# Kernel optimization log

Hardware: AMD Instinct MI355X
Metric: run time of the kernel (lower is better)

## Reference

```python
import jax, jax.numpy as jnp
import numpy as np

B, T_DIM, N, D, HID, NH = 2, 512, 6, 32, 128, 4
HD = HID // NH  # 32
GH = max(32, D)  # gater hidden = 32
FD = 128  # final_dim
EPS = 1e-5


def _ln(x, w, b):
    mu = jnp.mean(x, axis=-1, keepdims=True)
    var = jnp.var(x, axis=-1, keepdims=True)
    return (x - mu) * jax.lax.rsqrt(var + EPS) * w + b


def setup_inputs() -> dict:
    key = jax.random.key(0)
    ks = jax.random.split(key, 16)
    s_d = 1.0 / np.sqrt(D)
    s_h = 1.0 / np.sqrt(HID)
    s_g = 1.0 / np.sqrt(GH)
    return {
        "per_t_forces": jax.random.normal(ks[0], (B, T_DIM, N, D), jnp.float32),
        # gater: LayerNorm(D) -> Linear(D,GH) -> SiLU -> Linear(GH,1) (bias zero-init)
        "g_ln_w": jnp.ones((D,), jnp.float32),
        "g_ln_b": jnp.zeros((D,), jnp.float32),
        "g_w1": jax.random.uniform(ks[1], (D, GH), jnp.float32, -s_d, s_d),
        "g_b1": jax.random.uniform(ks[2], (GH,), jnp.float32, -s_d, s_d),
        "g_w2": jax.random.uniform(ks[3], (GH, 1), jnp.float32, -s_g, s_g),
        "g_b2": jnp.zeros((1,), jnp.float32),
        # QKV / out projections
        "q_w": jax.random.uniform(ks[4], (D, HID), jnp.float32, -s_d, s_d),
        "q_b": jax.random.uniform(ks[5], (HID,), jnp.float32, -s_d, s_d),
        "k_w": jax.random.uniform(ks[6], (D, HID), jnp.float32, -s_d, s_d),
        "k_b": jax.random.uniform(ks[7], (HID,), jnp.float32, -s_d, s_d),
        "v_w": jax.random.uniform(ks[8], (D, HID), jnp.float32, -s_d, s_d),
        "v_b": jax.random.uniform(ks[9], (HID,), jnp.float32, -s_d, s_d),
        "o_w": jax.random.uniform(ks[10], (HID, HID), jnp.float32, -s_h, s_h),
        "o_b": jax.random.uniform(ks[11], (HID,), jnp.float32, -s_h, s_h),
        # final: LayerNorm(HID) -> Linear(HID,FD) -> SiLU
        "f_ln_w": jnp.ones((HID,), jnp.float32),
        "f_ln_b": jnp.zeros((HID,), jnp.float32),
        "f_w": jax.random.uniform(ks[12], (HID, FD), jnp.float32, -s_h, s_h),
        "f_b": jax.random.uniform(ks[13], (FD,), jnp.float32, -s_h, s_h),
        "T": T_DIM,
    }


def reference(per_t_forces, g_ln_w, g_ln_b, g_w1, g_b1, g_w2, g_b2,
              q_w, q_b, k_w, k_b, v_w, v_b, o_w, o_b,
              f_ln_w, f_ln_b, f_w, f_b, T):
    b, tt, n, d = per_t_forces.shape
    L = T * n
    x = per_t_forces.reshape(b, L, d)

    # per-force learned gating
    h = jax.nn.silu(_ln(x, g_ln_w, g_ln_b) @ g_w1 + g_b1)
    gates = jax.nn.sigmoid((h @ g_w2 + g_b2)[..., 0])  # [B, L]
    g = gates[..., None]

    # gated QKV
    Q = (x @ q_w + q_b) * g
    K = (x @ k_w + k_b) * g
    V = (x @ v_w + v_b) * g

    Qh = Q.reshape(b, L, NH, HD)
    Kh = K.reshape(b, L, NH, HD)
    Vh = V.reshape(b, L, NH, HD)

    scale = 1.0 / np.sqrt(HD)
    scores = jnp.einsum("bihd,bjhd->bhij", Qh, Kh) * scale  # [B,NH,L,L]

    # block-causal over time: token j masked out if its time block > time of i
    t_idx = jnp.arange(L) // n
    mask = t_idx[None, :] > t_idx[:, None]  # [L, L], True = masked
    scores = jnp.where(mask[None, None], -jnp.inf, scores)

    A = jnp.maximum(jax.nn.softmax(scores, axis=-1), 1e-9)
    attn = jnp.einsum("bhij,bjhd->bihd", A, Vh).reshape(b, L, HID)

    out = attn @ o_w + o_b                     # [B, L, HID]
    per_t = out.reshape(b, T, n, HID).mean(axis=2)  # mean-pool over forces
    final = jax.nn.silu(_ln(per_t, f_ln_w, f_ln_b) @ f_w + f_b)  # [B, T, FD]
    return final
```

## Files before the change

### kernel.cpp

```cpp
#include <hip/hip_runtime.h>
#include <hip/hip_bf16.h>

#define BB   2
#define TT   512
#define NF   6
#define DD   32
#define HIDD 128
#define NHH  4
#define HDD  32
#define GHH  32
#define FDD  128
#define LL   (TT*NF)
#define EPSF 1e-5f
#define NQT16 (LL/16)

#define NCHC 8
#define CCH  384
#define VPAD 8

typedef __attribute__((ext_vector_type(8))) short  bf16x8;
typedef __attribute__((ext_vector_type(4))) float  f32x4;

#define MFMA16x16x32(a,b,c) __builtin_amdgcn_mfma_f32_16x16x32_bf16(a,b,c,0,0,0)

__device__ __forceinline__ unsigned short bfh(float f) {
    union { __hip_bfloat16 b; unsigned short u; } cv;
    cv.b = __float2bfloat16(f);
    return cv.u;
}
__device__ __forceinline__ float bff(unsigned short u) {
    return __uint_as_float(((unsigned)u) << 16);
}
__device__ __forceinline__ unsigned pk_bf16(float a, float b) {
    union { __hip_bfloat162 h2; unsigned u; } cv;
    cv.h2 = __float22bfloat162_rn(make_float2(a, b));
    return cv.u;
}
__device__ __forceinline__ bf16x8 ld8(const unsigned short* p) {
    return *reinterpret_cast<const bf16x8*>(p);
}

__device__ __forceinline__ float fexp2(float x) {
#if __has_builtin(__builtin_amdgcn_exp2f)
    return __builtin_amdgcn_exp2f(x);
#else
    return exp2f(x);
#endif
}

struct Frags {
    bf16x8 k0, k1;
    bf16x8 k2, k3;
    bf16x8 v0, v1, v2, v3;
};

__device__ __forceinline__ void load_tile_lds(
    const unsigned short* ldsK, const unsigned short* ldsV,
    int j0loc, int kloc0, int kloc1, int quad, int rr, Frags& f)
{
    const int kX0 = (j0loc + kloc0) * HDD + quad * 8;
    const int kX1 = (j0loc + kloc1) * HDD + quad * 8;
    f.k0 = ld8(ldsK + kX0);
    f.k1 = ld8(ldsK + kX1);
    f.k2 = ld8(ldsK + kX0 + 32 * HDD);
    f.k3 = ld8(ldsK + kX1 + 32 * HDD);
    const int vX = j0loc + quad * 8, vY = vX + 32;
    const int vr0 = rr * (CCH + VPAD), vr1 = (rr + 16) * (CCH + VPAD);
    f.v0 = ld8(ldsV + vr0 + vX);
    f.v1 = ld8(ldsV + vr1 + vX);
    f.v2 = ld8(ldsV + vr0 + vY);
    f.v3 = ld8(ldsV + vr1 + vY);
}

__device__ __forceinline__ void compute_tile(
    const Frags& f, const bf16x8 qfh, const bf16x8 qfl,
    int j0, int jminw, int jend, int quad,
    float& m, float& l, f32x4& o0, f32x4& o1)
{
    const f32x4 z = {0.f, 0.f, 0.f, 0.f};
    f32x4 s0 = MFMA16x16x32(f.k0, qfh, z);
    f32x4 s1 = MFMA16x16x32(f.k1, qfh, z);
    f32x4 s2 = MFMA16x16x32(f.k2, qfh, z);
    f32x4 s3 = MFMA16x16x32(f.k3, qfh, z);
    s0 = MFMA16x16x32(f.k0, qfl, s0);
    s1 = MFMA16x16x32(f.k1, qfl, s1);
    s2 = MFMA16x16x32(f.k2, qfl, s2);
    s3 = MFMA16x16x32(f.k3, qfl, s3);

    float e[16], mx, ls, corr;
    if (j0 + 64 <= jminw) {
        f32x4 m4 = s0;
        #pragma unroll
        for (int r2 = 0; r2 < 4; r2++)
            m4[r2] = fmaxf(fmaxf(m4[r2], s1[r2]), fmaxf(s2[r2], s3[r2]));
        mx = fmaxf(fmaxf(m4[0], m4[1]), fmaxf(m4[2], m4[3]));
        mx = fmaxf(mx, __shfl_xor(mx, 16));
        mx = fmaxf(mx, __shfl_xor(mx, 32));
        mx = fmaxf(m, mx);
        corr = fexp2(m - mx); m = mx;
        ls = 0.f;
        #pragma unroll
        for (int r2 = 0; r2 < 4; r2++) {
            float e0 = fexp2(s0[r2] - mx);
            float e1 = fexp2(s1[r2] - mx);
            float e2 = fexp2(s2[r2] - mx);
            float e3 = fexp2(s3[r2] - mx);
            e[r2] = e0; e[4 + r2] = e1; e[8 + r2] = e2; e[12 + r2] = e3;
            ls += (e0 + e1) + (e2 + e3);
        }
    } else {
        const int je = jend - j0;
        const int k0 = 8 * quad;
        float t[16];
        #pragma unroll
        for (int r2 = 0; r2 < 4; r2++) {
            t[r2]      = (k0 + r2          < je) ? s0[r2] : -1e30f;
            t[4 + r2]  = (k0 + 4 + r2      < je) ? s1[r2] : -1e30f;
            t[8 + r2]  = (32 + k0 + r2     < je) ? s2[r2] : -1e30f;
            t[12 + r2] = (32 + k0 + 4 + r2 < je) ? s3[r2] : -1e30f;
        }
        mx = t[0];
        #pragma unroll
        for (int i = 1; i < 16; i++) mx = fmaxf(mx, t[i]);
        mx = fmaxf(mx, __shfl_xor(mx, 16));
        mx = fmaxf(mx, __shfl_xor(mx, 32));
        mx = fmaxf(m, mx);
        corr = fexp2(m - mx); m = mx;
        ls = 0.f;
        #pragma unroll
        for (int r2 = 0; r2 < 4; r2++) {
            float e0 = fexp2(t[r2] - mx);
            float e1 = fexp2(t[4 + r2] - mx);
            float e2 = fexp2(t[8 + r2] - mx);
            float e3 = fexp2(t[12 + r2] - mx);
            e0 = (k0 + r2          < je) ? e0 : 0.f;
            e1 = (k0 + 4 + r2      < je) ? e1 : 0.f;
            e2 = (32 + k0 + r2     < je) ? e2 : 0.f;
            e3 = (32 + k0 + 4 + r2 < je) ? e3 : 0.f;
            e[r2] = e0; e[4 + r2] = e1; e[8 + r2] = e2; e[12 + r2] = e3;
            ls += (e0 + e1) + (e2 + e3);
        }
    }
    l = l * corr + ls;
    #pragma unroll
    for (int i = 0; i < 4; i++) { o0[i] *= corr; o1[i] *= corr; }

    union { unsigned u[4]; bf16x8 v; } pbX, pbY;
    pbX.u[0] = pk_bf16(e[0],  e[1]);
    pbX.u[1] = pk_bf16(e[2],  e[3]);
    pbX.u[2] = pk_bf16(e[4],  e[5]);
    pbX.u[3] = pk_bf16(e[6],  e[7]);
    pbY.u[0] = pk_bf16(e[8],  e[9]);
    pbY.u[1] = pk_bf16(e[10], e[11]);
    pbY.u[2] = pk_bf16(e[12], e[13]);
    pbY.u[3] = pk_bf16(e[14], e[15]);

    o0 = MFMA16x16x32(f.v0, pbX.v, o0);
    o1 = MFMA16x16x32(f.v1, pbX.v, o1);
    o0 = MFMA16x16x32(f.v2, pbY.v, o0);
    o1 = MFMA16x16x32(f.v3, pbY.v, o1);
}

__global__ __launch_bounds__(128) void gate_qkv_kernel(
    const float* __restrict__ x,
    const float* __restrict__ g_ln_w, const float* __restrict__ g_ln_b,
    const float* __restrict__ g_w1,   const float* __restrict__ g_b1,
    const float* __restrict__ g_w2,   const float* __restrict__ g_b2,
    const float* __restrict__ q_w,    const float* __restrict__ q_b,
    const float* __restrict__ k_w,    const float* __restrict__ k_b,
    const float* __restrict__ v_w,    const float* __restrict__ v_b,
    unsigned short* __restrict__ Qh, unsigned short* __restrict__ Ql,
    unsigned short* __restrict__ Kh,
    unsigned short* __restrict__ Vth)
{
    const int tok0 = blockIdx.x * 4;
    const int tid  = threadIdx.x;

    __shared__ float xs[4][DD];
    __shared__ float lns[4][DD];
    __shared__ float hs[4][GHH];
    __shared__ float gate_s[4];

    xs[tid >> 5][tid & 31] = x[(size_t)tok0 * DD + tid];
    __syncthreads();

    const int tk = (tid >> 5) & 1;
    const int d5 = tid & 31;
    if (tid < 64) {
        #pragma unroll
        for (int tt = 0; tt < 2; tt++) {
            int t = tt * 2 + tk;
            float xv = xs[t][d5];
            float s1 = xv, s2 = xv * xv;
            #pragma unroll
            for (int m = 16; m >= 1; m >>= 1) {
                s1 += __shfl_xor(s1, m, 32);
                s2 += __shfl_xor(s2, m, 32);
            }
            float mu  = s1 * (1.0f / DD);
            float var = s2 * (1.0f / DD) - mu * mu;
            float r   = rsqrtf(var + EPSF);
            lns[t][d5] = (xv - mu) * r * g_ln_w[d5] + g_ln_b[d5];
        }
    }
    __syncthreads();
    if (tid < 64) {
        #pragma unroll
        for (int tt = 0; tt < 2; tt++) {
            int t = tt * 2 + tk;
            float acc = g_b1[d5];
            #pragma unroll
            for (int d = 0; d < DD; d++) acc += lns[t][d] * g_w1[d * GHH + d5];
            hs[t][d5] = acc / (1.0f + __expf(-acc));
        }
    }
    __syncthreads();
    if (tid < 64) {
        #pragma unroll
        for (int tt = 0; tt < 2; tt++) {
            int t = tt * 2 + tk;
            float p = hs[t][d5] * g_w2[d5];
            #pragma unroll
            for (int m = 16; m >= 1; m >>= 1) p += __shfl_xor(p, m, 32);
            if (d5 == 0) gate_s[t] = 1.0f / (1.0f + __expf(-(p + g_b2[0])));
        }
    }
    __syncthreads();

    const int col = tid;
    float aq[4], ak[4], av[4];
    #pragma unroll
    for (int t = 0; t < 4; t++) { aq[t] = q_b[col]; ak[t] = k_b[col]; av[t] = v_b[col]; }
    #pragma unroll
    for (int d = 0; d < DD; d++) {
        float wq = q_w[d * HIDD + col];
        float wk = k_w[d * HIDD + col];
        float wv = v_w[d * HIDD + col];
        #pragma unroll
        for (int t = 0; t < 4; t++) {
            float xd = xs[t][d];
            aq[t] += xd * wq; ak[t] += xd * wk; av[t] += xd * wv;
        }
    }

    const int b    = tok0 / LL;
    const int l0   = tok0 - b * LL;
    const int head = col >> 5;
    const int d5c  = col & 31;
    const float scale = 0.25503486f;

    unsigned short vh[4];
    #pragma unroll
    for (int t = 0; t < 4; t++) {
        const float g = gate_s[t];
        const size_t a = ((size_t)(b * NHH + head) * LL + l0 + t) * HDD + d5c;
        float qv = aq[t] * g * scale;
        unsigned short h = bfh(qv); Qh[a] = h; Ql[a] = bfh(qv - bff(h));
        Kh[a] = bfh(ak[t] * g);
        vh[t] = bfh(av[t] * g);
    }
    const size_t vbase = ((size_t)(b * NHH + head) * HDD + d5c) * LL + l0;
    *(ushort4*)(Vth + vbase) = make_ushort4(vh[0], vh[1], vh[2], vh[3]);
}

__global__ __launch_bounds__(256) void attn_mfma(
    const unsigned short* __restrict__ Qh, const unsigned short* __restrict__ Ql,
    const unsigned short* __restrict__ Kh,
    const unsigned short* __restrict__ Vth,
    float* __restrict__ P)
{
    const int lin = blockIdx.x;
    const int bh  = lin & 7;
    const int jj  = lin >> 3;
    const int ch  = jj / (LL / 64);
    const int qt  = (LL / 64 - 1) - (jj % (LL / 64));
    const int j0c = CCH * ch;
    const int jmax_blk = ((qt * 64 + 63) / NF + 1) * NF;
    if (j0c >= jmax_blk) return;

    __shared__ __align__(16) unsigned short ldsK[CCH * HDD];
    __shared__ __align__(16) unsigned short ldsV[HDD * (CCH + VPAD)];

    const int tid = threadIdx.x;

    {
        const unsigned short* gK = Kh + ((size_t)bh * LL + j0c) * HDD;
        const unsigned short* gV = Vth + (size_t)bh * HDD * LL + j0c;
        const int r  = tid >> 3;
        const int c8 = tid & 7;
        #pragma unroll
        for (int it = 0; it < CCH / 64; it++) {
            const int uk = it * 256 + tid;
            *reinterpret_cast<bf16x8*>(&ldsK[uk * 8]) = ld8(gK + uk * 8);
            const int off = it * 64 + c8 * 8;
            *reinterpret_cast<bf16x8*>(&ldsV[r * (CCH + VPAD) + off]) =
                ld8(gV + (size_t)r * LL + off);
        }
    }
    __syncthreads();

    const int w    = tid >> 6;
    const int lane = tid & 63;
    const int rr   = lane & 15;
    const int quad = lane >> 4;

    const int ig0   = qt * 64 + w * 16;
    const int ig    = ig0 + rr;
    const int jend  = (ig / NF + 1) * NF;
    const int jmaxw = ((ig0 + 15) / NF + 1) * NF;
    const int jminw = (ig0 / NF + 1) * NF;

    const int kend = min(jmaxw - j0c, CCH);
    if (kend <= 0) return;

    const size_t qo = ((size_t)bh * LL + ig) * HDD + quad * 8;
    const bf16x8 qfh = ld8(Qh + qo);
    const bf16x8 qfl = ld8(Ql + qo);

    const int kloc0 = 8 * (rr >> 2) + (rr & 3);
    const int kloc1 = kloc0 + 4;

    f32x4 o0 = {0.f,0.f,0.f,0.f}, o1 = {0.f,0.f,0.f,0.f};
    float m = -1e30f, l = 0.f;

    const int ntile = (kend + 63) >> 6;

    Frags f0;
    load_tile_lds(ldsK, ldsV, 0, kloc0, kloc1, quad, rr, f0);
    for (int i = 0; i < ntile; i++) {
        const int j0 = j0c + (i << 6);
        if (i + 1 < ntile) {
            Frags f1;
            load_tile_lds(ldsK, ldsV, (i + 1) << 6, kloc0, kloc1, quad, rr, f1);
            compute_tile(f0, qfh, qfl, j0, jminw, jend, quad, m, l, o0, o1);
            f0 = f1;
        } else {
            compute_tile(f0, qfh, qfl, j0, jminw, jend, quad, m, l, o0, o1);
        }
    }

    l += __shfl_xor(l, 16);
    l += __shfl_xor(l, 32);

    float* dst = P + ((((size_t)bh * NQT16 + (ig0 >> 4)) * NCHC + ch) * 16 + rr) * 36;
    *(f32x4*)(dst + quad * 4)      = o0;
    *(f32x4*)(dst + 16 + quad * 4) = o1;
    if (quad == 0) { dst[32] = m; dst[33] = l; }
}

__global__ __launch_bounds__(128) void final_kernel(
    const float* __restrict__ P,
    const float* __restrict__ o_w,    const float* __restrict__ o_b,
    const float* __restrict__ f_ln_w, const float* __restrict__ f_ln_b,
    const float* __restrict__ f_w,    const float* __restrict__ f_b,
    float* __restrict__ out, int C, int NCH)
{
    const int t = blockIdx.x;
    const int b = blockIdx.y;
    const int d = threadIdx.x;
    const int h  = d >> 5;
    const int hd = d & 31;
    const int bh = b * NHH + h;

    __shared__ float ms[HIDD];
    __shared__ float lnbuf[HIDD];
    __shared__ float w1[2], w2[2];

    const int jmax = (t + 1) * NF;
    const int nch  = min(NCH, (jmax + C - 1) / C);

    float M[NF], L[NF], O[NF];
    #pragma unroll
    for (int f = 0; f < NF; f++) { M[f] = -1e30f; L[f] = 0.f; O[f] = 0.f; }

    for (int c = 0; c < nch; c++) {
        #pragma unroll
        for (int f = 0; f < NF; f++) {
            const int row = t * NF + f;
            const float* pr = P + ((((size_t)bh * NQT16 + (row >> 4)) * NCH + c)
                                   * 16 + (row & 15)) * 36;
            const float mc = pr[32], lc = pr[33], oc = pr[hd];
            const float mm = fmaxf(M[f], mc);
            const float sa = fexp2(M[f] - mm), sb = fexp2(mc - mm);
            O[f] = O[f] * sa + oc * sb;
            L[f] = L[f] * sa + lc * sb;
            M[f] = mm;
        }
    }
    float acc = 0.0f;
    #pragma unroll
    for (int f = 0; f < NF; f++) acc += O[f] / L[f];
    acc *= (1.0f / NF);
    ms[d] = acc;
    __syncthreads();

    float ov = o_b[d];
    for (int k = 0; k < HIDD; k++) ov += ms[k] * o_w[k * HIDD + d];

    float s1 = ov, s2 = ov * ov;
    #pragma unroll
    for (int m = 32; m >= 1; m >>= 1) { s1 += __shfl_xor(s1, m); s2 += __shfl_xor(s2, m); }
    if ((d & 63) == 0) { w1[d >> 6] = s1; w2[d >> 6] = s2; }
    __syncthreads();
    float S1 = w1[0] + w1[1], S2 = w2[0] + w2[1];
    float mu  = S1 * (1.0f / HIDD);
    float var = S2 * (1.0f / HIDD) - mu * mu;
    float r   = rsqrtf(var + EPSF);
    float lnv = (ov - mu) * r * f_ln_w[d] + f_ln_b[d];
    lnbuf[d] = lnv;
    __syncthreads();

    float fv = f_b[d];
    for (int k = 0; k < HIDD; k++) fv += lnbuf[k] * f_w[k * HIDD + d];
    fv = fv / (1.0f + __expf(-fv));

    out[((size_t)(b * TT + t)) * FDD + d] = fv;
}

extern "C" void kernel_launch(void* const* d_in, const int* in_sizes, int n_in,
                              void* d_out, int out_size, void* d_ws, size_t ws_size,
                              hipStream_t stream)
{
    const float* x      = (const float*)d_in[0];
    const float* g_ln_w = (const float*)d_in[1];
    const float* g_ln_b = (const float*)d_in[2];
    const float* g_w1   = (const float*)d_in[3];
    const float* g_b1   = (const float*)d_in[4];
    const float* g_w2   = (const float*)d_in[5];
    const float* g_b2   = (const float*)d_in[6];
    const float* q_w    = (const float*)d_in[7];
    const float* q_b    = (const float*)d_in[8];
    const float* k_w    = (const float*)d_in[9];
    const float* k_b    = (const float*)d_in[10];
    const float* v_w    = (const float*)d_in[11];
    const float* v_b    = (const float*)d_in[12];
    const float* o_w    = (const float*)d_in[13];
    const float* o_b    = (const float*)d_in[14];
    const float* f_ln_w = (const float*)d_in[15];
    const float* f_ln_b = (const float*)d_in[16];
    const float* f_w    = (const float*)d_in[17];
    const float* f_b    = (const float*)d_in[18];

    const size_t ntok = (size_t)BB * NHH * LL * HDD;
    unsigned short* Qh  = (unsigned short*)d_ws;
    unsigned short* Ql  = Qh  + ntok;
    unsigned short* Kh  = Ql  + ntok;
    unsigned short* Vth = Kh + 2 * ntok;
    float* Pw = (float*)(Vth + 2 * ntok);

    gate_qkv_kernel<<<(BB * LL) / 4, 128, 0, stream>>>(
        x, g_ln_w, g_ln_b, g_w1, g_b1, g_w2, g_b2,
        q_w, q_b, k_w, k_b, v_w, v_b, Qh, Ql, Kh, Vth);

    attn_mfma<<<(LL / 64) * NCHC * BB * NHH, 256, 0, stream>>>(
        Qh, Ql, Kh, Vth, Pw);

    final_kernel<<<dim3(TT, BB), 128, 0, stream>>>(
        Pw, o_w, o_b, f_ln_w, f_ln_b, f_w, f_b, (float*)d_out, CCH, NCHC);
}
```

Measured before the change: 140.4 us.

## Add lazy softmax rescale, batch 16 tokens per QKV block, split final accumulators

The attention softmax now skips the running-max update and rescale of the accumulators unless some lane's new max exceeds the old one by more than a threshold (a lazy rescale). The masked and unmasked tile paths are merged. The gate/QKV kernel handles 16 tokens per block instead of 4, so each weight load is reused across more tokens and the full block takes part in the gate computation. The final kernel splits its dot products into four independent accumulators for more instruction-level parallelism. The larger token batch raises register pressure and launches fewer blocks, and the lazy rescale allows exponentials up to 2^8 in bf16, which may affect accuracy.

Result: no change. 140.5 us (+0.1%).

```diff
diff --git a/kernel.cpp b/kernel.cpp
--- a/kernel.cpp
+++ b/kernel.cpp
@@ -18,6 +18,8 @@
 #define CCH  384
 #define VPAD 8
 
+#define TPB  16
+
 typedef __attribute__((ext_vector_type(8))) short  bf16x8;
 typedef __attribute__((ext_vector_type(4))) float  f32x4;
 
@@ -87,63 +89,59 @@
     s2 = MFMA16x16x32(f.k2, qfl, s2);
     s3 = MFMA16x16x32(f.k3, qfl, s3);
 
-    float e[16], mx, ls, corr;
-    if (j0 + 64 <= jminw) {
-        f32x4 m4 = s0;
-        #pragma unroll
-        for (int r2 = 0; r2 < 4; r2++)
-            m4[r2] = fmaxf(fmaxf(m4[r2], s1[r2]), fmaxf(s2[r2], s3[r2]));
-        mx = fmaxf(fmaxf(m4[0], m4[1]), fmaxf(m4[2], m4[3]));
-        mx = fmaxf(mx, __shfl_xor(mx, 16));
+    const bool interior = (j0 + 64 <= jminw);
+    const int  je = jend - j0;
+    const int  k0 = 8 * quad;
+
+    float t16[16];
+    if (interior) {
+        #pragma unroll
+        for (int r2 = 0; r2 < 4; r2++) {
+            t16[r2]      = s0[r2];
+            t16[4 + r2]  = s1[r2];
+            t16[8 + r2]  = s2[r2];
+            t16[12 + r2] = s3[r2];
+        }
+    } else {
+        #pragma unroll
+        for (int r2 = 0; r2 < 4; r2++) {
+            t16[r2]      = (k0 + r2          < je) ? s0[r2] : -1e30f;
+            t16[4 + r2]  = (k0 + 4 + r2      < je) ? s1[r2] : -1e30f;
+            t16[8 + r2]  = (32 + k0 + r2     < je) ? s2[r2] : -1e30f;
+            t16[12 + r2] = (32 + k0 + 4 + r2 < je) ? s3[r2] : -1e30f;
+        }
+    }
+
+    float lanemax = t16[0];
+    #pragma unroll
+    for (int i = 1; i < 16; i++) lanemax = fmaxf(lanemax, t16[i]);
+
+    if (!__all(lanemax - m <= 8.0f)) {
+        float mx = fmaxf(lanemax, __shfl_xor(lanemax, 16));
         mx = fmaxf(mx, __shfl_xor(mx, 32));
         mx = fmaxf(m, mx);
-        corr = fexp2(m - mx); m = mx;
-        ls = 0.f;
+        const float corr = fexp2(m - mx);
+        m = mx;
+        l *= corr;
+        #pragma unroll
+        for (int i = 0; i < 4; i++) { o0[i] *= corr; o1[i] *= corr; }
+    }
+
+    float e[16], ls = 0.f;
+    #pragma unroll
+    for (int i = 0; i < 16; i++) e[i] = fexp2(t16[i] - m);
+    if (!interior) {
         #pragma unroll
         for (int r2 = 0; r2 < 4; r2++) {
-            float e0 = fexp2(s0[r2] - mx);
-            float e1 = fexp2(s1[r2] - mx);
-            float e2 = fexp2(s2[r2] - mx);
-            float e3 = fexp2(s3[r2] - mx);
-            e[r2] = e0; e[4 + r2] = e1; e[8 + r2] = e2; e[12 + r2] = e3;
-            ls += (e0 + e1) + (e2 + e3);
-        }
-    } else {
-        const int je = jend - j0;
-        const int k0 = 8 * quad;
-        float t[16];
-        #pragma unroll
-        for (int r2 = 0; r2 < 4; r2++) {
-            t[r2]      = (k0 + r2          < je) ? s0[r2] : -1e30f;
-            t[4 + r2]  = (k0 + 4 + r2      < je) ? s1[r2] : -1e30f;
-            t[8 + r2]  = (32 + k0 + r2     < je) ? s2[r2] : -1e30f;
-            t[12 + r2] = (32 + k0 + 4 + r2 < je) ? s3[r2] : -1e30f;
-        }
-        mx = t[0];
-        #pragma unroll
-        for (int i = 1; i < 16; i++) mx = fmaxf(mx, t[i]);
-        mx = fmaxf(mx, __shfl_xor(mx, 16));
-        mx = fmaxf(mx, __shfl_xor(mx, 32));
-        mx = fmaxf(m, mx);
-        corr = fexp2(m - mx); m = mx;
-        ls = 0.f;
-        #pragma unroll
-        for (int r2 = 0; r2 < 4; r2++) {
-            float e0 = fexp2(t[r2] - mx);
-            float e1 = fexp2(t[4 + r2] - mx);
-            float e2 = fexp2(t[8 + r2] - mx);
-            float e3 = fexp2(t[12 + r2] - mx);
-            e0 = (k0 + r2          < je) ? e0 : 0.f;
-            e1 = (k0 + 4 + r2      < je) ? e1 : 0.f;
-            e2 = (32 + k0 + r2     < je) ? e2 : 0.f;
-            e3 = (32 + k0 + 4 + r2 < je) ? e3 : 0.f;
-            e[r2] = e0; e[4 + r2] = e1; e[8 + r2] = e2; e[12 + r2] = e3;
-            ls += (e0 + e1) + (e2 + e3);
-        }
-    }
-    l = l * corr + ls;
-    #pragma unroll
-    for (int i = 0; i < 4; i++) { o0[i] *= corr; o1[i] *= corr; }
+            if (!(k0 + r2          < je)) e[r2]      = 0.f;
+            if (!(k0 + 4 + r2      < je)) e[4 + r2]  = 0.f;
+            if (!(32 + k0 + r2     < je)) e[8 + r2]  = 0.f;
+            if (!(32 + k0 + 4 + r2 < je)) e[12 + r2] = 0.f;
+        }
+    }
+    #pragma unroll
+    for (int i = 0; i < 16; i++) ls += e[i];
+    l += ls;
 
     union { unsigned u[4]; bf16x8 v; } pbX, pbY;
     pbX.u[0] = pk_bf16(e[0],  e[1]);
@@ -173,73 +171,79 @@
     unsigned short* __restrict__ Kh,
     unsigned short* __restrict__ Vth)
 {
-    const int tok0 = blockIdx.x * 4;
+    const int tok0 = blockIdx.x * TPB;
     const int tid  = threadIdx.x;
 
-    __shared__ float xs[4][DD];
-    __shared__ float lns[4][DD];
-    __shared__ float hs[4][GHH];
-    __shared__ float gate_s[4];
-
-    xs[tid >> 5][tid & 31] = x[(size_t)tok0 * DD + tid];
-    __syncthreads();
-
-    const int tk = (tid >> 5) & 1;
+    __shared__ float xs[TPB][DD];
+    __shared__ float lns[TPB][DD];
+    __shared__ float gate_s[TPB];
+
+    #pragma unroll
+    for (int i = 0; i < (TPB * DD) / 128; i++) {
+        const int idx = i * 128 + tid;
+        xs[idx >> 5][idx & 31] = x[(size_t)tok0 * DD + idx];
+    }
+    __syncthreads();
+
+    const int tg = tid >> 5;
     const int d5 = tid & 31;
-    if (tid < 64) {
-        #pragma unroll
-        for (int tt = 0; tt < 2; tt++) {
-            int t = tt * 2 + tk;
-            float xv = xs[t][d5];
-            float s1 = xv, s2 = xv * xv;
-            #pragma unroll
-            for (int m = 16; m >= 1; m >>= 1) {
-                s1 += __shfl_xor(s1, m, 32);
-                s2 += __shfl_xor(s2, m, 32);
-            }
-            float mu  = s1 * (1.0f / DD);
-            float var = s2 * (1.0f / DD) - mu * mu;
-            float r   = rsqrtf(var + EPSF);
-            lns[t][d5] = (xv - mu) * r * g_ln_w[d5] + g_ln_b[d5];
-        }
-    }
-    __syncthreads();
-    if (tid < 64) {
-        #pragma unroll
-        for (int tt = 0; tt < 2; tt++) {
-            int t = tt * 2 + tk;
-            float acc = g_b1[d5];
-            #pragma unroll
-            for (int d = 0; d < DD; d++) acc += lns[t][d] * g_w1[d * GHH + d5];
-            hs[t][d5] = acc / (1.0f + __expf(-acc));
-        }
-    }
-    __syncthreads();
-    if (tid < 64) {
-        #pragma unroll
-        for (int tt = 0; tt < 2; tt++) {
-            int t = tt * 2 + tk;
-            float p = hs[t][d5] * g_w2[d5];
-            #pragma unroll
-            for (int m = 16; m >= 1; m >>= 1) p += __shfl_xor(p, m, 32);
-            if (d5 == 0) gate_s[t] = 1.0f / (1.0f + __expf(-(p + g_b2[0])));
-        }
+
+    #pragma unroll
+    for (int tt = 0; tt < TPB / 4; tt++) {
+        const int t = tt * 4 + tg;
+        float xv = xs[t][d5];
+        float s1 = xv, s2 = xv * xv;
+        #pragma unroll
+        for (int mm = 16; mm >= 1; mm >>= 1) {
+            s1 += __shfl_xor(s1, mm, 32);
+            s2 += __shfl_xor(s2, mm, 32);
+        }
+        float mu  = s1 * (1.0f / DD);
+        float var = s2 * (1.0f / DD) - mu * mu;
+        float r   = rsqrtf(var + EPSF);
+        lns[t][d5] = (xv - mu) * r * g_ln_w[d5] + g_ln_b[d5];
+    }
+    __syncthreads();
+
+    #pragma unroll
+    for (int tt = 0; tt < TPB / 4; tt++) {
+        const int t = tt * 4 + tg;
+        float acc = g_b1[d5];
+        #pragma unroll
+        for (int d = 0; d < DD; d++) acc += lns[t][d] * g_w1[d * GHH + d5];
+        const float h = acc / (1.0f + __expf(-acc));
+        float p = h * g_w2[d5];
+        #pragma unroll
+        for (int mm = 16; mm >= 1; mm >>= 1) p += __shfl_xor(p, mm, 32);
+        if (d5 == 0) gate_s[t] = 1.0f / (1.0f + __expf(-(p + g_b2[0])));
     }
     __syncthreads();
 
     const int col = tid;
-    float aq[4], ak[4], av[4];
-    #pragma unroll
-    for (int t = 0; t < 4; t++) { aq[t] = q_b[col]; ak[t] = k_b[col]; av[t] = v_b[col]; }
-    #pragma unroll
-    for (int d = 0; d < DD; d++) {
-        float wq = q_w[d * HIDD + col];
-        float wk = k_w[d * HIDD + col];
-        float wv = v_w[d * HIDD + col];
-        #pragma unroll
-        for (int t = 0; t < 4; t++) {
-            float xd = xs[t][d];
-            aq[t] += xd * wq; ak[t] += xd * wk; av[t] += xd * wv;
+    float aq[TPB], ak[TPB], av[TPB];
+    {
+        const float qb = q_b[col], kb = k_b[col], vb = v_b[col];
+        #pragma unroll
+        for (int t = 0; t < TPB; t++) { aq[t] = qb; ak[t] = kb; av[t] = vb; }
+    }
+    for (int d4 = 0; d4 < DD / 4; d4++) {
+        float wq[4], wk[4], wv[4];
+        #pragma unroll
+        for (int j = 0; j < 4; j++) {
+            const int d = d4 * 4 + j;
+            wq[j] = q_w[d * HIDD + col];
+            wk[j] = k_w[d * HIDD + col];
+            wv[j] = v_w[d * HIDD + col];
+        }
+        #pragma unroll
+        for (int t = 0; t < TPB; t++) {
+            const float4 xv = *reinterpret_cast<const float4*>(&xs[t][d4 * 4]);
+            aq[t] += xv.x * wq[0]; aq[t] += xv.y * wq[1];
+            aq[t] += xv.z * wq[2]; aq[t] += xv.w * wq[3];
+            ak[t] += xv.x * wk[0]; ak[t] += xv.y * wk[1];
+            ak[t] += xv.z * wk[2]; ak[t] += xv.w * wk[3];
+            av[t] += xv.x * wv[0]; av[t] += xv.y * wv[1];
+            av[t] += xv.z * wv[2]; av[t] += xv.w * wv[3];
         }
     }
 
@@ -249,18 +253,20 @@
     const int d5c  = col & 31;
     const float scale = 0.25503486f;
 
-    unsigned short vh[4];
-    #pragma unroll
-    for (int t = 0; t < 4; t++) {
+    union { unsigned short s[TPB]; bf16x8 v8[TPB / 8]; } vh;
+    #pragma unroll
+    for (int t = 0; t < TPB; t++) {
         const float g = gate_s[t];
         const size_t a = ((size_t)(b * NHH + head) * LL + l0 + t) * HDD + d5c;
         float qv = aq[t] * g * scale;
         unsigned short h = bfh(qv); Qh[a] = h; Ql[a] = bfh(qv - bff(h));
         Kh[a] = bfh(ak[t] * g);
-        vh[t] = bfh(av[t] * g);
+        vh.s[t] = bfh(av[t] * g);
     }
     const size_t vbase = ((size_t)(b * NHH + head) * HDD + d5c) * LL + l0;
-    *(ushort4*)(Vth + vbase) = make_ushort4(vh[0], vh[1], vh[2], vh[3]);
+    #pragma unroll
+    for (int j = 0; j < TPB / 8; j++)
+        *reinterpret_cast<bf16x8*>(Vth + vbase + j * 8) = vh.v8[j];
 }
 
 __global__ __launch_bounds__(256) void attn_mfma(
@@ -394,8 +400,14 @@
     ms[d] = acc;
     __syncthreads();
 
-    float ov = o_b[d];
-    for (int k = 0; k < HIDD; k++) ov += ms[k] * o_w[k * HIDD + d];
+    float ov0 = 0.f, ov1 = 0.f, ov2 = 0.f, ov3 = 0.f;
+    for (int k = 0; k < HIDD; k += 4) {
+        ov0 += ms[k]     * o_w[(k)     * HIDD + d];
+        ov1 += ms[k + 1] * o_w[(k + 1) * HIDD + d];
+        ov2 += ms[k + 2] * o_w[(k + 2) * HIDD + d];
+        ov3 += ms[k + 3] * o_w[(k + 3) * HIDD + d];
+    }
+    float ov = o_b[d] + ((ov0 + ov1) + (ov2 + ov3));
 
     float s1 = ov, s2 = ov * ov;
     #pragma unroll
@@ -410,8 +422,14 @@
     lnbuf[d] = lnv;
     __syncthreads();
 
-    float fv = f_b[d];
-    for (int k = 0; k < HIDD; k++) fv += lnbuf[k] * f_w[k * HIDD + d];
+    float fv0 = 0.f, fv1 = 0.f, fv2 = 0.f, fv3 = 0.f;
+    for (int k = 0; k < HIDD; k += 4) {
+        fv0 += lnbuf[k]     * f_w[(k)     * HIDD + d];
+        fv1 += lnbuf[k + 1] * f_w[(k + 1) * HIDD + d];
+        fv2 += lnbuf[k + 2] * f_w[(k + 2) * HIDD + d];
+        fv3 += lnbuf[k + 3] * f_w[(k + 3) * HIDD + d];
+    }
+    float fv = f_b[d] + ((fv0 + fv1) + (fv2 + fv3));
     fv = fv / (1.0f + __expf(-fv));
 
     out[((size_t)(b * TT + t)) * FDD + d] = fv;
@@ -448,7 +466,7 @@
     unsigned short* Vth = Kh + 2 * ntok;
     float* Pw = (float*)(Vth + 2 * ntok);
 
-    gate_qkv_kernel<<<(BB * LL) / 4, 128, 0, stream>>>(
+    gate_qkv_kernel<<<(BB * LL) / TPB, 128, 0, stream>>>(
         x, g_ln_w, g_ln_b, g_w1, g_b1, g_w2, g_b2,
         q_w, q_b, k_w, k_b, v_w, v_b, Qh, Ql, Kh, Vth);
 
```
